# Kernel tuning notes

Hardware: AMD Instinct MI355X
Metric: run time of the kernel (lower is better)

The kernel has to match this reference:

```python
import jax, jax.numpy as jnp
import numpy as np

IN_CH, OUT_CH = 384, 512


def setup_inputs() -> dict:
    key = jax.random.key(0)
    ks = jax.random.split(key, 9)
    B, C, H, W = 8, IN_CH, 48, 48
    s_in = 1.0 / np.sqrt(IN_CH)
    s_out = 1.0 / np.sqrt(OUT_CH)
    return {
        "x": jax.random.normal(ks[0], (B, C, H, W), dtype=jnp.float32),
        "Wq": jax.random.uniform(ks[1], (OUT_CH, IN_CH), jnp.float32, -s_in, s_in),
        "bq": jax.random.uniform(ks[2], (OUT_CH,), jnp.float32, -s_in, s_in),
        "Wk": jax.random.uniform(ks[3], (OUT_CH, IN_CH), jnp.float32, -s_in, s_in),
        "bk": jax.random.uniform(ks[4], (OUT_CH,), jnp.float32, -s_in, s_in),
        "Wv": jax.random.uniform(ks[5], (OUT_CH, IN_CH), jnp.float32, -s_in, s_in),
        "bv": jax.random.uniform(ks[6], (OUT_CH,), jnp.float32, -s_in, s_in),
        "Wo": jax.random.uniform(ks[7], (OUT_CH, OUT_CH), jnp.float32, -s_out, s_out),
        "bo": jax.random.uniform(ks[8], (OUT_CH,), jnp.float32, -s_out, s_out),
    }


def reference(x, Wq, bq, Wk, bk, Wv, bv, Wo, bo):
    B, C, H, W = x.shape
    N = H * W  # number of spatial tokens
    xf = x.reshape(B, C, N)  # [B, C, N]
    # 1x1 convs == per-pixel linear projections
    q = jnp.einsum('oc,bcn->bno', Wq, xf) + bq  # [B, N, O]
    k = jnp.einsum('oc,bcn->bon', Wk, xf) + bk[None, :, None]  # [B, O, N]
    v = jnp.einsum('oc,bcn->bon', Wv, xf) + bv[None, :, None]  # [B, O, N]
    scale = 1.0 / jnp.sqrt(jnp.asarray(Wq.shape[0], x.dtype))
    attn = jax.nn.softmax(jnp.einsum('bno,bom->bnm', q, k) * scale, axis=-1)  # [B, N, N]
    out = jnp.einsum('bom,bnm->bon', v, attn)  # [B, O, N]
    out = jnp.einsum('po,bon->bpn', Wo, out) + bo[None, :, None]
    return out.reshape(B, Wo.shape[0], H, W)
```

## Files before the change

kernel.cpp:

```cpp
#include <hip/hip_runtime.h>
#include <stdint.h>

#define B_    8
#define CIN   384
#define OCH   512
#define NTOK  2304
#define SCALE 0.044194173824159216f

typedef unsigned short u16;
typedef u16   u16x8 __attribute__((ext_vector_type(8)));
typedef short s16x8 __attribute__((ext_vector_type(8)));
typedef float f32x4 __attribute__((ext_vector_type(4)));

__device__ __forceinline__ u16 f2bf(float f) {
    union { uint32_t i; float f; } v; v.f = f;
    uint32_t r = v.i + 0x7fffu + ((v.i >> 16) & 1u);
    return (u16)(r >> 16);
}

typedef __attribute__((address_space(1))) const uint32_t glb_u32;
typedef __attribute__((address_space(3))) uint32_t lds_u32;

__device__ __forceinline__ size_t baddr(int row, int col, int Kc) {
    return ((size_t)(row >> 4) * (Kc >> 5) + (col >> 5)) * 512
         + (size_t)(((col >> 3) & 3) * 128 + (row & 15) * 8 + (col & 7));
}

__device__ __forceinline__ void stage64(const u16* __restrict__ pA, size_t rs,
                                        u16* __restrict__ dst, int w)
{
    u16* lp = dst + w * 1024;
    __builtin_amdgcn_global_load_lds((glb_u32*)pA,              (lds_u32*)lp,           16, 0, 0);
    __builtin_amdgcn_global_load_lds((glb_u32*)(pA + rs),       (lds_u32*)(lp + 512),   16, 0, 0);
    __builtin_amdgcn_global_load_lds((glb_u32*)(pA + 512),      (lds_u32*)(lp + 4096),  16, 0, 0);
    __builtin_amdgcn_global_load_lds((glb_u32*)(pA + rs + 512), (lds_u32*)(lp + 4608),  16, 0, 0);
}

__device__ __forceinline__ void mfma_core(const u16* __restrict__ As,
                                          const u16* __restrict__ Bs,
                                          int wm16, int wn16, int lrow, int kq,
                                          f32x4 acc[4][4])
{
    s16x8 a[4], b[4];
#pragma unroll
    for (int i = 0; i < 4; ++i)
        a[i] = *(const s16x8*)(As + (((wm16 + i) * 64) + kq * 16 + lrow) * 8);
#pragma unroll
    for (int j = 0; j < 4; ++j)
        b[j] = *(const s16x8*)(Bs + (((wn16 + j) * 64) + kq * 16 + lrow) * 8);
#pragma unroll
    for (int i = 0; i < 4; ++i)
#pragma unroll
        for (int j = 0; j < 4; ++j)
            acc[i][j] = __builtin_amdgcn_mfma_f32_16x16x32_bf16(a[i], b[j], acc[i][j], 0, 0, 0);
}

#define KLOOP64(Abase, Bbase, m0_, n0_, K_)                                    \
    {                                                                          \
        const size_t rs_ = (size_t)((K_) >> 5) * 512;                          \
        const u16* pA_ = (Abase)                                               \
            + (size_t)((((m0_) >> 4) + w * 2) * ((K_) >> 5)) * 512             \
            + (size_t)ln * 8;                                                  \
        const u16* pB_ = (Bbase)                                               \
            + (size_t)((((n0_) >> 4) + w * 2) * ((K_) >> 5)) * 512             \
            + (size_t)ln * 8;                                                  \
        for (int k0_ = 0; k0_ < (K_); k0_ += 64) {                             \
            stage64(pA_, rs_, As, w);                                          \
            stage64(pB_, rs_, Bs, w);                                          \
            __syncthreads();                                                   \
            mfma_core(As, Bs, wm16, wn16, lrow, kq, acc);                      \
            mfma_core(As + 4096, Bs + 4096, wm16, wn16, lrow, kq, acc);        \
            __syncthreads();                                                   \
            pA_ += 1024; pB_ += 1024;                                          \
        }                                                                      \
    }

#define WQKV_SZ (OCH * CIN)
#define WO_SZ   (OCH * OCH)
#define CH_QKV  (WQKV_SZ / 8)
#define CH_WO   (WO_SZ / 8)
#define CH_TOT  (3 * CH_QKV + CH_WO)

__global__ __launch_bounds__(256) void prep_w_kernel(
    const float* __restrict__ Wq, const float* __restrict__ Wk,
    const float* __restrict__ Wv, const float* __restrict__ Wo,
    u16* __restrict__ Wqb, u16* __restrict__ Wkb,
    u16* __restrict__ Wvb, u16* __restrict__ Wob)
{
    int lc = blockIdx.x * 256 + threadIdx.x;
    if (lc >= CH_TOT) return;
    const float* src; u16* dst; int Kc;
    if      (lc < CH_QKV)     { src = Wq; dst = Wqb; Kc = CIN; }
    else if (lc < 2 * CH_QKV) { src = Wk; dst = Wkb; Kc = CIN; lc -= CH_QKV; }
    else if (lc < 3 * CH_QKV) { src = Wv; dst = Wvb; Kc = CIN; lc -= 2 * CH_QKV; }
    else                      { src = Wo; dst = Wob; Kc = OCH; lc -= 3 * CH_QKV; }
    const int brick = lc >> 6, l = lc & 63;
    const int bpr = Kc >> 5;
    const int g = brick / bpr, c = brick % bpr;
    const int row = g * 16 + (l & 15);
    const int col = c * 32 + (l >> 4) * 8;
    const float* s = src + (size_t)row * Kc + col;
    float4 v0 = *(const float4*)s;
    float4 v1 = *(const float4*)(s + 4);
    u16x8 o;
    o[0] = f2bf(v0.x); o[1] = f2bf(v0.y); o[2] = f2bf(v0.z); o[3] = f2bf(v0.w);
    o[4] = f2bf(v1.x); o[5] = f2bf(v1.y); o[6] = f2bf(v1.z); o[7] = f2bf(v1.w);
    *(u16x8*)(dst + (size_t)lc * 8) = o;
}

__global__ __launch_bounds__(256) void transpose_x_kernel(
    const float* __restrict__ x, u16* __restrict__ xT)
{
    const int n0 = blockIdx.x * 64;
    const int c0 = blockIdx.y * 64;
    const int b  = blockIdx.z;
    const float* X = x + (size_t)b * CIN * NTOK;

    __shared__ float Ts[64][66];

    const int t = threadIdx.x;
#pragma unroll
    for (int rep = 0; rep < 4; ++rep) {
        const int cr = (t >> 4) + rep * 16;
        const int n4 = (t & 15) * 4;
        float4 v = *(const float4*)(X + (size_t)(c0 + cr) * NTOK + n0 + n4);
        *(float2*)&Ts[cr][n4]     = make_float2(v.x, v.y);
        *(float2*)&Ts[cr][n4 + 2] = make_float2(v.z, v.w);
    }
    __syncthreads();

    u16* O = xT + (size_t)b * NTOK * CIN;
#pragma unroll
    for (int rep = 0; rep < 2; ++rep) {
        const int nr = (t >> 3) + rep * 32;
        const int c8 = (t & 7) * 8;
        u16 tmp[8];
#pragma unroll
        for (int j = 0; j < 8; ++j) tmp[j] = f2bf(Ts[c8 + j][nr]);
        *(u16x8*)(O + baddr(n0 + nr, c0 + c8, CIN)) = *(const u16x8*)tmp;
    }
}

__global__ __launch_bounds__(256) void qk_kernel(
    const u16* __restrict__ xT,
    const u16* __restrict__ Wqb, const float* __restrict__ bq,
    const u16* __restrict__ Wkb, const float* __restrict__ bk,
    u16* __restrict__ Qt, u16* __restrict__ Kt)
{
    const int zz  = blockIdx.x % 16;
    const int b   = zz & 7, which = zz >> 3;
    const int rem = blockIdx.x / 16;
    const int n0 = (rem % 4) * 128;
    const int m0 = (rem / 4) * 128;
    const u16* A  = xT + (size_t)b * NTOK * CIN;
    const u16* Bp = which ? Wkb : Wqb;
    const float* bias = which ? bk : bq;
    u16* C = (which ? Kt : Qt) + (size_t)b * NTOK * OCH;

    __shared__ u16 As[8192];
    __shared__ u16 Bs[8192];

    const int t = threadIdx.x;
    const int w = t >> 6, ln = t & 63;
    const int wm16 = (w & 1) * 4, wn16 = (w >> 1) * 4;
    const int lrow = ln & 15, kq = ln >> 4;

    f32x4 acc[4][4] = {};

    KLOOP64(A, Bp, m0, n0, CIN)

    const int offl = ((lrow >> 3) << 7) + (lrow & 7) + (kq << 5);
    float bcol[4];
#pragma unroll
    for (int j = 0; j < 4; ++j)
        bcol[j] = bias[n0 + (wn16 + j) * 16 + lrow];
#pragma unroll
    for (int i = 0; i < 4; ++i) {
        u16* Crow = C + ((size_t)((m0 >> 4) + wm16 + i) * (OCH >> 5) + (n0 >> 5)) * 512 + offl;
#pragma unroll
        for (int j = 0; j < 4; ++j) {
            u16* Cj = Crow + ((wn16 + j) >> 1) * 512 + ((j & 1) << 8);
#pragma unroll
            for (int r = 0; r < 4; ++r)
                Cj[r * 8] = f2bf(acc[i][j][r] + bcol[j]);
        }
    }
}

template <int BIAS, typename OutT>
__global__ __launch_bounds__(256) void gemm_kernel(
    const u16* __restrict__ Ag, const u16* __restrict__ Bg,
    const float* __restrict__ bias, OutT* __restrict__ Cg,
    int K, int N, long sA, long sB, long sC, int GX, int GZ)
{
    const int z   = blockIdx.x % GZ;
    const int rem = blockIdx.x / GZ;
    const int n0 = (rem % GX) * 128;
    const int m0 = (rem / GX) * 128;
    const u16* A  = Ag + (size_t)z * sA;
    const u16* Bp = Bg + (size_t)z * sB;
    OutT* C = Cg + (size_t)z * sC;

    __shared__ u16 As[8192];
    __shared__ u16 Bs[8192];

    const int t = threadIdx.x;
    const int w = t >> 6, ln = t & 63;
    const int wm16 = (w & 1) * 4, wn16 = (w >> 1) * 4;
    const int lrow = ln & 15, kq = ln >> 4;

    f32x4 acc[4][4] = {};

    KLOOP64(A, Bp, m0, n0, K)

    if constexpr (sizeof(OutT) == 2) {
        const int offl = ((lrow >> 3) << 7) + (lrow & 7) + (kq << 5);
#pragma unroll
        for (int i = 0; i < 4; ++i) {
            float4 b4 = make_float4(0.f, 0.f, 0.f, 0.f);
            if (BIAS == 1)
                b4 = *(const float4*)(bias + m0 + (wm16 + i) * 16 + kq * 4);
            u16* Crow = (u16*)C + ((size_t)((m0 >> 4) + wm16 + i) * (N >> 5) + (n0 >> 5)) * 512 + offl;
#pragma unroll
            for (int j = 0; j < 4; ++j) {
                u16* Cj = Crow + ((wn16 + j) >> 1) * 512 + ((j & 1) << 8);
                Cj[0]  = f2bf(acc[i][j][0] + b4.x);
                Cj[8]  = f2bf(acc[i][j][1] + b4.y);
                Cj[16] = f2bf(acc[i][j][2] + b4.z);
                Cj[24] = f2bf(acc[i][j][3] + b4.w);
            }
        }
    } else {
#pragma unroll
        for (int i = 0; i < 4; ++i) {
            const int row = m0 + (wm16 + i) * 16 + kq * 4;
#pragma unroll
            for (int r = 0; r < 4; ++r) {
                float badd = 0.f;
                if (BIAS == 1) badd = bias[row + r];
#pragma unroll
                for (int j = 0; j < 4; ++j) {
                    const int col = n0 + (wn16 + j) * 16 + lrow;
                    C[(size_t)(row + r) * N + col] = acc[i][j][r] + badd;
                }
            }
        }
    }
}

__global__ __launch_bounds__(256) void logits_exp_kernel(
    const u16* __restrict__ Qt, const u16* __restrict__ Kt,
    u16* __restrict__ Ew, float* __restrict__ rowsumG)
{
    const int z   = blockIdx.x % B_;
    const int rem = blockIdx.x / B_;
    const int n0 = (rem % (NTOK / 128)) * 128;
    const int m0 = (rem / (NTOK / 128)) * 128;
    const u16* A  = Qt + (size_t)z * NTOK * OCH;
    const u16* Bp = Kt + (size_t)z * NTOK * OCH;

    __shared__ u16 As[8192];
    __shared__ u16 Bs[8192];
    __shared__ float rowsumL[128];

    const int t = threadIdx.x;
    const int w = t >> 6, ln = t & 63;
    const int wm16 = (w & 1) * 4, wn16 = (w >> 1) * 4;
    const int lrow = ln & 15, kq = ln >> 4;

    if (t < 128) rowsumL[t] = 0.f;

    f32x4 acc[4][4] = {};

    KLOOP64(A, Bp, m0, n0, OCH)

    u16* E = Ew + (size_t)z * NTOK * NTOK;
    const int offl = ((lrow >> 3) << 7) + (lrow & 7) + (kq << 5);
#pragma unroll
    for (int i = 0; i < 4; ++i) {
        u16* Erow = E + ((size_t)((m0 >> 4) + wm16 + i) * (NTOK >> 5) + (n0 >> 5)) * 512 + offl;
#pragma unroll
        for (int r = 0; r < 4; ++r) {
            float part = 0.f;
#pragma unroll
            for (int j = 0; j < 4; ++j) {
                float e = __expf(acc[i][j][r] * SCALE);
                part += e;
                Erow[((wn16 + j) >> 1) * 512 + ((j & 1) << 8) + r * 8] = f2bf(e);
            }
            part += __shfl_xor(part, 1);
            part += __shfl_xor(part, 2);
            part += __shfl_xor(part, 4);
            part += __shfl_xor(part, 8);
            if (lrow == 0) atomicAdd(&rowsumL[(wm16 + i) * 16 + kq * 4 + r], part);
        }
    }
    __syncthreads();
    if (t < 128) atomicAdd(&rowsumG[(size_t)z * NTOK + m0 + t], rowsumL[t]);
}

__global__ __launch_bounds__(256) void pv_div_kernel(
    const u16* __restrict__ Ew, const u16* __restrict__ Vw,
    const float* __restrict__ rowsumG, u16* __restrict__ AOt)
{
    const int z   = blockIdx.x % B_;
    const int rem = blockIdx.x / B_;
    const int n0 = (rem % 4) * 128;
    const int m0 = (rem / 4) * 128;
    const u16* A  = Ew + (size_t)z * NTOK * NTOK;
    const u16* Bp = Vw + (size_t)z * OCH * NTOK;

    __shared__ u16 As[8192];
    __shared__ u16 Bs[8192];

    const int t = threadIdx.x;
    const int w = t >> 6, ln = t & 63;
    const int wm16 = (w & 1) * 4, wn16 = (w >> 1) * 4;
    const int lrow = ln & 15, kq = ln >> 4;

    f32x4 acc[4][4] = {};

    KLOOP64(A, Bp, m0, n0, NTOK)

    u16* AO = AOt + (size_t)z * NTOK * OCH;
    const int offl = ((lrow >> 3) << 7) + (lrow & 7) + (kq << 5);
#pragma unroll
    for (int i = 0; i < 4; ++i) {
        const float4 rs4 = *(const float4*)(rowsumG + (size_t)z * NTOK + m0 + (wm16 + i) * 16 + kq * 4);
        const float inv0 = 1.0f / rs4.x, inv1 = 1.0f / rs4.y;
        const float inv2 = 1.0f / rs4.z, inv3 = 1.0f / rs4.w;
        u16* Crow = AO + ((size_t)((m0 >> 4) + wm16 + i) * (OCH >> 5) + (n0 >> 5)) * 512 + offl;
#pragma unroll
        for (int j = 0; j < 4; ++j) {
            u16* Cj = Crow + ((wn16 + j) >> 1) * 512 + ((j & 1) << 8);
            Cj[0]  = f2bf(acc[i][j][0] * inv0);
            Cj[8]  = f2bf(acc[i][j][1] * inv1);
            Cj[16] = f2bf(acc[i][j][2] * inv2);
            Cj[24] = f2bf(acc[i][j][3] * inv3);
        }
    }
}

extern "C" void kernel_launch(void* const* d_in, const int* in_sizes, int n_in,
                              void* d_out, int out_size, void* d_ws, size_t ws_size,
                              hipStream_t stream)
{
    const float* x  = (const float*)d_in[0];
    const float* Wq = (const float*)d_in[1];
    const float* bq = (const float*)d_in[2];
    const float* Wk = (const float*)d_in[3];
    const float* bk = (const float*)d_in[4];
    const float* Wv = (const float*)d_in[5];
    const float* bv = (const float*)d_in[6];
    const float* Wo = (const float*)d_in[7];
    const float* bo = (const float*)d_in[8];
    float* out = (float*)d_out;

    u16* ws = (u16*)d_ws;
    u16* Wqb = ws;
    u16* Wkb = Wqb + WQKV_SZ;
    u16* Wvb = Wkb + WQKV_SZ;
    u16* Wob = Wvb + WQKV_SZ;
    u16* xT  = Wob + WO_SZ;
    const size_t xtsz  = (size_t)B_ * NTOK * CIN;
    const size_t qkvsz = (size_t)B_ * NTOK * OCH;
    u16* Qt  = xT + xtsz;
    u16* Kt  = Qt + qkvsz;
    u16* Vw  = Kt + qkvsz;
    u16* Ew  = Vw + qkvsz;
    float* rowsumG = (float*)(Ew + (size_t)B_ * NTOK * NTOK);
    u16* AOt = Qt;

    dim3 blk(256);

    prep_w_kernel<<<dim3((CH_TOT + 255) / 256), blk, 0, stream>>>(
        Wq, Wk, Wv, Wo, Wqb, Wkb, Wvb, Wob);
    transpose_x_kernel<<<dim3(NTOK / 64, CIN / 64, B_), blk, 0, stream>>>(x, xT);
    hipMemsetAsync(rowsumG, 0, (size_t)B_ * NTOK * sizeof(float), stream);

    qk_kernel<<<dim3(4 * 18 * 16), blk, 0, stream>>>(
        xT, Wqb, bq, Wkb, bk, Qt, Kt);
    gemm_kernel<1, u16><<<dim3(18 * 4 * B_), blk, 0, stream>>>(
        Wvb, xT, bv, Vw, CIN, NTOK, 0L, (long)NTOK * CIN, (long)OCH * NTOK, 18, B_);

    logits_exp_kernel<<<dim3(18 * 18 * B_), blk, 0, stream>>>(Qt, Kt, Ew, rowsumG);

    pv_div_kernel<<<dim3(4 * 18 * B_), blk, 0, stream>>>(Ew, Vw, rowsumG, AOt);

    gemm_kernel<1, float><<<dim3(18 * 4 * B_), blk, 0, stream>>>(
        Wob, AOt, bo, out, OCH, NTOK, 0L, (long)NTOK * OCH, (long)OCH * NTOK, 18, B_);
}
```

Before: 325.9 us.

## Replace 128x128 4-wave GEMMs with single-wave 64x64 double-buffered pipelined tiles

Every GEMM stage now uses a single-wave 64-thread block computing a 64x64 tile. Tiles are staged through two LDS buffers with direct global-to-LDS loads and manual vmcnt waits, so the next K-slice loads while the current one runs on MFMA, with no __syncthreads. The Q, K and V projections are merged into one launch, and the logits kernel atomically adds row sums straight to global memory instead of reducing them in shared memory first. The aim is to hide load latency and remove barrier cost, at the price of less data reuse per tile, more global traffic and more atomics.

```diff
diff --git a/kernel.cpp b/kernel.cpp
--- a/kernel.cpp
+++ b/kernel.cpp
@@ -21,19 +21,13 @@
 typedef __attribute__((address_space(1))) const uint32_t glb_u32;
 typedef __attribute__((address_space(3))) uint32_t lds_u32;
 
+__device__ __forceinline__ void gld16(const u16* g, u16* l) {
+    __builtin_amdgcn_global_load_lds((glb_u32*)g, (lds_u32*)l, 16, 0, 0);
+}
+
 __device__ __forceinline__ size_t baddr(int row, int col, int Kc) {
     return ((size_t)(row >> 4) * (Kc >> 5) + (col >> 5)) * 512
          + (size_t)(((col >> 3) & 3) * 128 + (row & 15) * 8 + (col & 7));
-}
-
-__device__ __forceinline__ void stage64(const u16* __restrict__ pA, size_t rs,
-                                        u16* __restrict__ dst, int w)
-{
-    u16* lp = dst + w * 1024;
-    __builtin_amdgcn_global_load_lds((glb_u32*)pA,              (lds_u32*)lp,           16, 0, 0);
-    __builtin_amdgcn_global_load_lds((glb_u32*)(pA + rs),       (lds_u32*)(lp + 512),   16, 0, 0);
-    __builtin_amdgcn_global_load_lds((glb_u32*)(pA + 512),      (lds_u32*)(lp + 4096),  16, 0, 0);
-    __builtin_amdgcn_global_load_lds((glb_u32*)(pA + rs + 512), (lds_u32*)(lp + 4608),  16, 0, 0);
 }
 
 __device__ __forceinline__ void mfma_core(const u16* __restrict__ As,
@@ -55,25 +49,141 @@
             acc[i][j] = __builtin_amdgcn_mfma_f32_16x16x32_bf16(a[i], b[j], acc[i][j], 0, 0, 0);
 }
 
-#define KLOOP64(Abase, Bbase, m0_, n0_, K_)                                    \
-    {                                                                          \
-        const size_t rs_ = (size_t)((K_) >> 5) * 512;                          \
-        const u16* pA_ = (Abase)                                               \
-            + (size_t)((((m0_) >> 4) + w * 2) * ((K_) >> 5)) * 512             \
-            + (size_t)ln * 8;                                                  \
-        const u16* pB_ = (Bbase)                                               \
-            + (size_t)((((n0_) >> 4) + w * 2) * ((K_) >> 5)) * 512             \
-            + (size_t)ln * 8;                                                  \
-        for (int k0_ = 0; k0_ < (K_); k0_ += 64) {                             \
-            stage64(pA_, rs_, As, w);                                          \
-            stage64(pB_, rs_, Bs, w);                                          \
-            __syncthreads();                                                   \
-            mfma_core(As, Bs, wm16, wn16, lrow, kq, acc);                      \
-            mfma_core(As + 4096, Bs + 4096, wm16, wn16, lrow, kq, acc);        \
-            __syncthreads();                                                   \
-            pA_ += 1024; pB_ += 1024;                                          \
-        }                                                                      \
-    }
+template <int MODE, int K>
+__device__ __forceinline__ void gemm64_core(
+    u16* __restrict__ sm,
+    const u16* __restrict__ A, const u16* __restrict__ Bp,
+    const float* __restrict__ aux, void* __restrict__ Cout,
+    int N, int m0, int n0, float* __restrict__ rsG)
+{
+    constexpr int NT = K / 32;
+    u16* As0 = sm;
+    u16* Bs0 = sm + 2048;
+    u16* As1 = sm + 4096;
+    u16* Bs1 = sm + 6144;
+
+    const int ln = threadIdx.x & 63;
+    const int lrow = ln & 15, kq = ln >> 4;
+
+    const int bpr = K >> 5;
+    const size_t rstep = (size_t)bpr << 9;
+    const u16* pA = A  + (((size_t)(m0 >> 4) * bpr) << 9) + (size_t)(ln << 3);
+    const u16* pB = Bp + (((size_t)(n0 >> 4) * bpr) << 9) + (size_t)(ln << 3);
+
+    f32x4 acc[4][4] = {};
+
+#define STAGE8(ga, gb, Ad, Bd)                                             \
+    gld16((ga),             (Ad));        gld16((ga) + rstep,     (Ad) + 512);  \
+    gld16((ga) + 2 * rstep, (Ad) + 1024); gld16((ga) + 3 * rstep, (Ad) + 1536); \
+    gld16((gb),             (Bd));        gld16((gb) + rstep,     (Bd) + 512);  \
+    gld16((gb) + 2 * rstep, (Bd) + 1024); gld16((gb) + 3 * rstep, (Bd) + 1536);
+
+    STAGE8(pA, pB, As0, Bs0)
+
+#pragma unroll 1
+    for (int kt = 0; kt < NT; kt += 2) {
+        STAGE8(pA + 512, pB + 512, As1, Bs1)
+        asm volatile("s_waitcnt vmcnt(8)" ::: "memory");
+        mfma_core(As0, Bs0, 0, 0, lrow, kq, acc);
+        asm volatile("" ::: "memory");
+        if (kt + 2 < NT) {
+            STAGE8(pA + 1024, pB + 1024, As0, Bs0)
+            asm volatile("s_waitcnt vmcnt(8)" ::: "memory");
+        } else {
+            asm volatile("s_waitcnt vmcnt(0)" ::: "memory");
+        }
+        mfma_core(As1, Bs1, 0, 0, lrow, kq, acc);
+        asm volatile("" ::: "memory");
+        pA += 1024; pB += 1024;
+    }
+#undef STAGE8
+
+    const int offl = ((lrow >> 3) << 7) + (lrow & 7) + (kq << 5);
+
+    if constexpr (MODE == 0) {
+        u16* E = (u16*)Cout;
+#pragma unroll
+        for (int i = 0; i < 4; ++i) {
+            u16* Erow = E + ((size_t)((m0 >> 4) + i) * (N >> 5) + (n0 >> 5)) * 512 + offl;
+#pragma unroll
+            for (int r = 0; r < 4; ++r) {
+                float part = 0.f;
+#pragma unroll
+                for (int j = 0; j < 4; ++j) {
+                    float e = __expf(acc[i][j][r] * SCALE);
+                    part += e;
+                    Erow[(j >> 1) * 512 + ((j & 1) << 8) + r * 8] = f2bf(e);
+                }
+                part += __shfl_xor(part, 1);
+                part += __shfl_xor(part, 2);
+                part += __shfl_xor(part, 4);
+                part += __shfl_xor(part, 8);
+                if (lrow == 0) atomicAdd(&rsG[m0 + i * 16 + kq * 4 + r], part);
+            }
+        }
+    } else if constexpr (MODE == 1) {
+        u16* C = (u16*)Cout;
+        float bcol[4];
+#pragma unroll
+        for (int j = 0; j < 4; ++j) bcol[j] = aux[n0 + j * 16 + lrow];
+#pragma unroll
+        for (int i = 0; i < 4; ++i) {
+            u16* Crow = C + ((size_t)((m0 >> 4) + i) * (N >> 5) + (n0 >> 5)) * 512 + offl;
+#pragma unroll
+            for (int j = 0; j < 4; ++j) {
+                u16* Cj = Crow + (j >> 1) * 512 + ((j & 1) << 8);
+#pragma unroll
+                for (int r = 0; r < 4; ++r)
+                    Cj[r * 8] = f2bf(acc[i][j][r] + bcol[j]);
+            }
+        }
+    } else if constexpr (MODE == 2) {
+        u16* C = (u16*)Cout;
+#pragma unroll
+        for (int i = 0; i < 4; ++i) {
+            const float4 b4 = *(const float4*)(aux + m0 + i * 16 + kq * 4);
+            u16* Crow = C + ((size_t)((m0 >> 4) + i) * (N >> 5) + (n0 >> 5)) * 512 + offl;
+#pragma unroll
+            for (int j = 0; j < 4; ++j) {
+                u16* Cj = Crow + (j >> 1) * 512 + ((j & 1) << 8);
+                Cj[0]  = f2bf(acc[i][j][0] + b4.x);
+                Cj[8]  = f2bf(acc[i][j][1] + b4.y);
+                Cj[16] = f2bf(acc[i][j][2] + b4.z);
+                Cj[24] = f2bf(acc[i][j][3] + b4.w);
+            }
+        }
+    } else if constexpr (MODE == 3) {
+        u16* C = (u16*)Cout;
+#pragma unroll
+        for (int i = 0; i < 4; ++i) {
+            const float4 rs4 = *(const float4*)(aux + m0 + i * 16 + kq * 4);
+            const float inv0 = 1.0f / rs4.x, inv1 = 1.0f / rs4.y;
+            const float inv2 = 1.0f / rs4.z, inv3 = 1.0f / rs4.w;
+            u16* Crow = C + ((size_t)((m0 >> 4) + i) * (N >> 5) + (n0 >> 5)) * 512 + offl;
+#pragma unroll
+            for (int j = 0; j < 4; ++j) {
+                u16* Cj = Crow + (j >> 1) * 512 + ((j & 1) << 8);
+                Cj[0]  = f2bf(acc[i][j][0] * inv0);
+                Cj[8]  = f2bf(acc[i][j][1] * inv1);
+                Cj[16] = f2bf(acc[i][j][2] * inv2);
+                Cj[24] = f2bf(acc[i][j][3] * inv3);
+            }
+        }
+    } else {
+        float* C = (float*)Cout;
+#pragma unroll
+        for (int i = 0; i < 4; ++i) {
+            const int row = m0 + i * 16 + kq * 4;
+            const float4 b4 = *(const float4*)(aux + row);
+            const float bv4[4] = {b4.x, b4.y, b4.z, b4.w};
+#pragma unroll
+            for (int r = 0; r < 4; ++r)
+#pragma unroll
+                for (int j = 0; j < 4; ++j)
+                    C[(size_t)(row + r) * N + n0 + j * 16 + lrow] = acc[i][j][r] + bv4[r];
+        }
+    }
+}
 
 #define WQKV_SZ (OCH * CIN)
 #define WO_SZ   (OCH * OCH)
@@ -141,204 +251,64 @@
     }
 }
 
-__global__ __launch_bounds__(256) void qk_kernel(
+__global__ __launch_bounds__(64) void qkv64_kernel(
     const u16* __restrict__ xT,
     const u16* __restrict__ Wqb, const float* __restrict__ bq,
     const u16* __restrict__ Wkb, const float* __restrict__ bk,
-    u16* __restrict__ Qt, u16* __restrict__ Kt)
-{
-    const int zz  = blockIdx.x % 16;
-    const int b   = zz & 7, which = zz >> 3;
-    const int rem = blockIdx.x / 16;
-    const int n0 = (rem % 4) * 128;
-    const int m0 = (rem / 4) * 128;
-    const u16* A  = xT + (size_t)b * NTOK * CIN;
-    const u16* Bp = which ? Wkb : Wqb;
-    const float* bias = which ? bk : bq;
-    u16* C = (which ? Kt : Qt) + (size_t)b * NTOK * OCH;
-
-    __shared__ u16 As[8192];
-    __shared__ u16 Bs[8192];
-
-    const int t = threadIdx.x;
-    const int w = t >> 6, ln = t & 63;
-    const int wm16 = (w & 1) * 4, wn16 = (w >> 1) * 4;
-    const int lrow = ln & 15, kq = ln >> 4;
-
-    f32x4 acc[4][4] = {};
-
-    KLOOP64(A, Bp, m0, n0, CIN)
-
-    const int offl = ((lrow >> 3) << 7) + (lrow & 7) + (kq << 5);
-    float bcol[4];
-#pragma unroll
-    for (int j = 0; j < 4; ++j)
-        bcol[j] = bias[n0 + (wn16 + j) * 16 + lrow];
-#pragma unroll
-    for (int i = 0; i < 4; ++i) {
-        u16* Crow = C + ((size_t)((m0 >> 4) + wm16 + i) * (OCH >> 5) + (n0 >> 5)) * 512 + offl;
-#pragma unroll
-        for (int j = 0; j < 4; ++j) {
-            u16* Cj = Crow + ((wn16 + j) >> 1) * 512 + ((j & 1) << 8);
-#pragma unroll
-            for (int r = 0; r < 4; ++r)
-                Cj[r * 8] = f2bf(acc[i][j][r] + bcol[j]);
-        }
-    }
-}
-
-template <int BIAS, typename OutT>
-__global__ __launch_bounds__(256) void gemm_kernel(
-    const u16* __restrict__ Ag, const u16* __restrict__ Bg,
-    const float* __restrict__ bias, OutT* __restrict__ Cg,
-    int K, int N, long sA, long sB, long sC, int GX, int GZ)
-{
-    const int z   = blockIdx.x % GZ;
-    const int rem = blockIdx.x / GZ;
-    const int n0 = (rem % GX) * 128;
-    const int m0 = (rem / GX) * 128;
-    const u16* A  = Ag + (size_t)z * sA;
-    const u16* Bp = Bg + (size_t)z * sB;
-    OutT* C = Cg + (size_t)z * sC;
-
-    __shared__ u16 As[8192];
-    __shared__ u16 Bs[8192];
-
-    const int t = threadIdx.x;
-    const int w = t >> 6, ln = t & 63;
-    const int wm16 = (w & 1) * 4, wn16 = (w >> 1) * 4;
-    const int lrow = ln & 15, kq = ln >> 4;
-
-    f32x4 acc[4][4] = {};
-
-    KLOOP64(A, Bp, m0, n0, K)
-
-    if constexpr (sizeof(OutT) == 2) {
-        const int offl = ((lrow >> 3) << 7) + (lrow & 7) + (kq << 5);
-#pragma unroll
-        for (int i = 0; i < 4; ++i) {
-            float4 b4 = make_float4(0.f, 0.f, 0.f, 0.f);
-            if (BIAS == 1)
-                b4 = *(const float4*)(bias + m0 + (wm16 + i) * 16 + kq * 4);
-            u16* Crow = (u16*)C + ((size_t)((m0 >> 4) + wm16 + i) * (N >> 5) + (n0 >> 5)) * 512 + offl;
-#pragma unroll
-            for (int j = 0; j < 4; ++j) {
-                u16* Cj = Crow + ((wn16 + j) >> 1) * 512 + ((j & 1) << 8);
-                Cj[0]  = f2bf(acc[i][j][0] + b4.x);
-                Cj[8]  = f2bf(acc[i][j][1] + b4.y);
-                Cj[16] = f2bf(acc[i][j][2] + b4.z);
-                Cj[24] = f2bf(acc[i][j][3] + b4.w);
-            }
-        }
+    const u16* __restrict__ Wvb, const float* __restrict__ bv,
+    u16* __restrict__ Qt, u16* __restrict__ Kt, u16* __restrict__ Vw)
+{
+    __shared__ __align__(16) u16 sm[8192];
+    const int sel = blockIdx.x % 24;
+    const int b = sel & 7, which = sel >> 3;
+    const int rem = blockIdx.x / 24;
+    const u16* xTb = xT + (size_t)b * NTOK * CIN;
+    if (which < 2) {
+        const int n0 = (rem & 7) * 64, m0 = (rem >> 3) * 64;
+        gemm64_core<1, CIN>(sm, xTb, which ? Wkb : Wqb, which ? bk : bq,
+            (which ? Kt : Qt) + (size_t)b * NTOK * OCH, OCH, m0, n0, nullptr);
     } else {
-#pragma unroll
-        for (int i = 0; i < 4; ++i) {
-            const int row = m0 + (wm16 + i) * 16 + kq * 4;
-#pragma unroll
-            for (int r = 0; r < 4; ++r) {
-                float badd = 0.f;
-                if (BIAS == 1) badd = bias[row + r];
-#pragma unroll
-                for (int j = 0; j < 4; ++j) {
-                    const int col = n0 + (wn16 + j) * 16 + lrow;
-                    C[(size_t)(row + r) * N + col] = acc[i][j][r] + badd;
-                }
-            }
-        }
-    }
-}
-
-__global__ __launch_bounds__(256) void logits_exp_kernel(
+        const int n0 = (rem % 36) * 64, m0 = (rem / 36) * 64;
+        gemm64_core<2, CIN>(sm, Wvb, xTb, bv,
+            Vw + (size_t)b * OCH * NTOK, NTOK, m0, n0, nullptr);
+    }
+}
+
+__global__ __launch_bounds__(64) void logits64_kernel(
     const u16* __restrict__ Qt, const u16* __restrict__ Kt,
     u16* __restrict__ Ew, float* __restrict__ rowsumG)
 {
-    const int z   = blockIdx.x % B_;
-    const int rem = blockIdx.x / B_;
-    const int n0 = (rem % (NTOK / 128)) * 128;
-    const int m0 = (rem / (NTOK / 128)) * 128;
-    const u16* A  = Qt + (size_t)z * NTOK * OCH;
-    const u16* Bp = Kt + (size_t)z * NTOK * OCH;
-
-    __shared__ u16 As[8192];
-    __shared__ u16 Bs[8192];
-    __shared__ float rowsumL[128];
-
-    const int t = threadIdx.x;
-    const int w = t >> 6, ln = t & 63;
-    const int wm16 = (w & 1) * 4, wn16 = (w >> 1) * 4;
-    const int lrow = ln & 15, kq = ln >> 4;
-
-    if (t < 128) rowsumL[t] = 0.f;
-
-    f32x4 acc[4][4] = {};
-
-    KLOOP64(A, Bp, m0, n0, OCH)
-
-    u16* E = Ew + (size_t)z * NTOK * NTOK;
-    const int offl = ((lrow >> 3) << 7) + (lrow & 7) + (kq << 5);
-#pragma unroll
-    for (int i = 0; i < 4; ++i) {
-        u16* Erow = E + ((size_t)((m0 >> 4) + wm16 + i) * (NTOK >> 5) + (n0 >> 5)) * 512 + offl;
-#pragma unroll
-        for (int r = 0; r < 4; ++r) {
-            float part = 0.f;
-#pragma unroll
-            for (int j = 0; j < 4; ++j) {
-                float e = __expf(acc[i][j][r] * SCALE);
-                part += e;
-                Erow[((wn16 + j) >> 1) * 512 + ((j & 1) << 8) + r * 8] = f2bf(e);
-            }
-            part += __shfl_xor(part, 1);
-            part += __shfl_xor(part, 2);
-            part += __shfl_xor(part, 4);
-            part += __shfl_xor(part, 8);
-            if (lrow == 0) atomicAdd(&rowsumL[(wm16 + i) * 16 + kq * 4 + r], part);
-        }
-    }
-    __syncthreads();
-    if (t < 128) atomicAdd(&rowsumG[(size_t)z * NTOK + m0 + t], rowsumL[t]);
-}
-
-__global__ __launch_bounds__(256) void pv_div_kernel(
+    __shared__ __align__(16) u16 sm[8192];
+    const int z = blockIdx.x & 7;
+    const int rem = blockIdx.x >> 3;
+    const int n0 = (rem % 36) * 64, m0 = (rem / 36) * 64;
+    gemm64_core<0, OCH>(sm, Qt + (size_t)z * NTOK * OCH, Kt + (size_t)z * NTOK * OCH,
+        nullptr, Ew + (size_t)z * NTOK * NTOK, NTOK, m0, n0,
+        rowsumG + (size_t)z * NTOK);
+}
+
+__global__ __launch_bounds__(64) void pv64_kernel(
     const u16* __restrict__ Ew, const u16* __restrict__ Vw,
     const float* __restrict__ rowsumG, u16* __restrict__ AOt)
 {
-    const int z   = blockIdx.x % B_;
-    const int rem = blockIdx.x / B_;
-    const int n0 = (rem % 4) * 128;
-    const int m0 = (rem / 4) * 128;
-    const u16* A  = Ew + (size_t)z * NTOK * NTOK;
-    const u16* Bp = Vw + (size_t)z * OCH * NTOK;
-
-    __shared__ u16 As[8192];
-    __shared__ u16 Bs[8192];
-
-    const int t = threadIdx.x;
-    const int w = t >> 6, ln = t & 63;
-    const int wm16 = (w & 1) * 4, wn16 = (w >> 1) * 4;
-    const int lrow = ln & 15, kq = ln >> 4;
-
-    f32x4 acc[4][4] = {};
-
-    KLOOP64(A, Bp, m0, n0, NTOK)
-
-    u16* AO = AOt + (size_t)z * NTOK * OCH;
-    const int offl = ((lrow >> 3) << 7) + (lrow & 7) + (kq << 5);
-#pragma unroll
-    for (int i = 0; i < 4; ++i) {
-        const float4 rs4 = *(const float4*)(rowsumG + (size_t)z * NTOK + m0 + (wm16 + i) * 16 + kq * 4);
-        const float inv0 = 1.0f / rs4.x, inv1 = 1.0f / rs4.y;
-        const float inv2 = 1.0f / rs4.z, inv3 = 1.0f / rs4.w;
-        u16* Crow = AO + ((size_t)((m0 >> 4) + wm16 + i) * (OCH >> 5) + (n0 >> 5)) * 512 + offl;
-#pragma unroll
-        for (int j = 0; j < 4; ++j) {
-            u16* Cj = Crow + ((wn16 + j) >> 1) * 512 + ((j & 1) << 8);
-            Cj[0]  = f2bf(acc[i][j][0] * inv0);
-            Cj[8]  = f2bf(acc[i][j][1] * inv1);
-            Cj[16] = f2bf(acc[i][j][2] * inv2);
-            Cj[24] = f2bf(acc[i][j][3] * inv3);
-        }
-    }
+    __shared__ __align__(16) u16 sm[8192];
+    const int z = blockIdx.x & 7;
+    const int rem = blockIdx.x >> 3;
+    const int n0 = (rem & 7) * 64, m0 = (rem >> 3) * 64;
+    gemm64_core<3, NTOK>(sm, Ew + (size_t)z * NTOK * NTOK, Vw + (size_t)z * OCH * NTOK,
+        rowsumG + (size_t)z * NTOK, AOt + (size_t)z * NTOK * OCH, OCH, m0, n0, nullptr);
+}
+
+__global__ __launch_bounds__(64) void out64_kernel(
+    const u16* __restrict__ Wob, const u16* __restrict__ AOt,
+    const float* __restrict__ bo, float* __restrict__ out)
+{
+    __shared__ __align__(16) u16 sm[8192];
+    const int z = blockIdx.x & 7;
+    const int rem = blockIdx.x >> 3;
+    const int n0 = (rem % 36) * 64, m0 = (rem / 36) * 64;
+    gemm64_core<4, OCH>(sm, Wob, AOt + (size_t)z * NTOK * OCH, bo,
+        out + (size_t)z * OCH * NTOK, NTOK, m0, n0, nullptr);
 }
 
 extern "C" void kernel_launch(void* const* d_in, const int* in_sizes, int n_in,
@@ -371,22 +341,19 @@
     float* rowsumG = (float*)(Ew + (size_t)B_ * NTOK * NTOK);
     u16* AOt = Qt;
 
-    dim3 blk(256);
+    dim3 blk(256), blk64(64);
 
     prep_w_kernel<<<dim3((CH_TOT + 255) / 256), blk, 0, stream>>>(
         Wq, Wk, Wv, Wo, Wqb, Wkb, Wvb, Wob);
     transpose_x_kernel<<<dim3(NTOK / 64, CIN / 64, B_), blk, 0, stream>>>(x, xT);
     hipMemsetAsync(rowsumG, 0, (size_t)B_ * NTOK * sizeof(float), stream);
 
-    qk_kernel<<<dim3(4 * 18 * 16), blk, 0, stream>>>(
-        xT, Wqb, bq, Wkb, bk, Qt, Kt);
-    gemm_kernel<1, u16><<<dim3(18 * 4 * B_), blk, 0, stream>>>(
-        Wvb, xT, bv, Vw, CIN, NTOK, 0L, (long)NTOK * CIN, (long)OCH * NTOK, 18, B_);
-
-    logits_exp_kernel<<<dim3(18 * 18 * B_), blk, 0, stream>>>(Qt, Kt, Ew, rowsumG);
-
-    pv_div_kernel<<<dim3(4 * 18 * B_), blk, 0, stream>>>(Ew, Vw, rowsumG, AOt);
-
-    gemm_kernel<1, float><<<dim3(18 * 4 * B_), blk, 0, stream>>>(
-        Wob, AOt, bo, out, OCH, NTOK, 0L, (long)NTOK * OCH, (long)OCH * NTOK, 18, B_);
-}
+    qkv64_kernel<<<dim3(288 * 24), blk64, 0, stream>>>(
+        xT, Wqb, bq, Wkb, bk, Wvb, bv, Qt, Kt, Vw);
+
+    logits64_kernel<<<dim3(1296 * 8), blk64, 0, stream>>>(Qt, Kt, Ew, rowsumG);
+
+    pv64_kernel<<<dim3(288 * 8), blk64, 0, stream>>>(Ew, Vw, rowsumG, AOt);
+
+    out64_kernel<<<dim3(288 * 8), blk64, 0, stream>>>(Wob, AOt, bo, out);
+}
```

New measurement: 295.2 us. 1.1x faster.
